# Performance work log

Measured on AMD Instinct MI355X. Metric: run time of the kernel, lower is better.

Reference implementation:

```python
import jax, jax.numpy as jnp
import numpy as np

N, E, DIN, DOUT = 50000, 800000, 256, 64
LN_EPS = 1e-5


def setup_inputs() -> dict:
    key = jax.random.key(0)
    k1, k2, k3 = jax.random.split(key, 3)
    xs = jax.random.normal(k1, (N, DIN), dtype=jnp.float32)
    edge_index = jax.random.randint(k2, (2, E), 0, N, dtype=jnp.int64)
    # GCNConv linear weight (glorot-ish) and bias
    W = jax.random.normal(k3, (DOUT, DIN), dtype=jnp.float32) * (1.0 / np.sqrt(DIN))
    b = jnp.zeros((DOUT,), dtype=jnp.float32)
    # LayerNorm affine params
    gamma = jnp.ones((DOUT,), dtype=jnp.float32)
    beta = jnp.zeros((DOUT,), dtype=jnp.float32)
    return {"xs": xs, "edge_index": edge_index, "W": W, "b": b, "gamma": gamma, "beta": beta}


def reference(xs, edge_index, W, b, gamma, beta):
    n = xs.shape[0]
    # 1) linear transform first (PyG GCNConv order): [N, DOUT]
    h = xs @ W.T
    # 2) add self loops
    loop = jnp.arange(n, dtype=edge_index.dtype)
    src = jnp.concatenate([edge_index[0], loop])
    dst = jnp.concatenate([edge_index[1], loop])
    # 3) symmetric normalization: deg over destinations (incl. self loops)
    deg = jax.ops.segment_sum(jnp.ones_like(dst, dtype=h.dtype), dst, num_segments=n)
    dinv = jnp.where(deg > 0, jax.lax.rsqrt(deg), 0.0)
    norm = dinv[src] * dinv[dst]  # [E+N]
    # 4) gather -> weight -> scatter-add
    msg = h[src] * norm[:, None]  # [E+N, DOUT]
    out = jax.ops.segment_sum(msg, dst, num_segments=n) + b
    # 5) LayerNorm over feature dim
    mu = jnp.mean(out, axis=-1, keepdims=True)
    var = jnp.mean(jnp.square(out - mu), axis=-1, keepdims=True)
    return (out - mu) * jax.lax.rsqrt(var + LN_EPS) * gamma + beta
```

## Files before the change

kernel.cpp:

```cpp
#include <hip/hip_runtime.h>

#define N_NODES 50000
#define N_EDGES 800000
#define DIN 256
#define DOUT 64
#define LN_EPS 1e-5f
#define NB 782
#define BCAP 2048
#define EPB 2048

typedef __attribute__((ext_vector_type(8))) short bfrag8;
typedef __attribute__((ext_vector_type(4))) float f32x4;

__device__ inline unsigned short f2bf(float f) {
    unsigned u = __builtin_bit_cast(unsigned, f);
    u += 0x7fffu + ((u >> 16) & 1u);
    return (unsigned short)(u >> 16);
}
__device__ inline float bf2f(unsigned short b) {
    unsigned u = ((unsigned)b) << 16;
    return __builtin_bit_cast(float, u);
}

__global__ void zero_gcur_kernel(int* __restrict__ gcur) {
    int i = blockIdx.x * 256 + threadIdx.x;
    if (i < NB) gcur[i] = 0;
}

__global__ __launch_bounds__(512) void partition_kernel(
    const int* __restrict__ ei, int* __restrict__ gcur, unsigned* __restrict__ bdata) {
    __shared__ int hist[NB];
    __shared__ int hbase[NB];
    const int tid = threadIdx.x;
    for (int c = tid; c < NB; c += 512) hist[c] = 0;
    __syncthreads();
    const int chunk = blockIdx.x * EPB;
    unsigned u[4];
    int bk[4];
    int rk[4];
    #pragma unroll
    for (int i = 0; i < 4; ++i) {
        int e = chunk + i * 512 + tid;
        if (e < N_EDGES) {
            int s = ei[e];
            int d = ei[N_EDGES + e];
            u[i] = (unsigned)s | ((unsigned)(d & 63) << 17);
            bk[i] = d >> 6;
            rk[i] = atomicAdd(&hist[bk[i]], 1);
        } else { bk[i] = -1; u[i] = 0; rk[i] = 0; }
    }
    __syncthreads();
    for (int c = tid; c < NB; c += 512) {
        int n = hist[c];
        hbase[c] = n ? atomicAdd(&gcur[c], n) : 0;
    }
    __syncthreads();
    #pragma unroll
    for (int i = 0; i < 4; ++i) {
        if (bk[i] >= 0) {
            int off = hbase[bk[i]] + rk[i];
            if (off < BCAP) bdata[(size_t)bk[i] * BCAP + off] = u[i];
        }
    }
}

__global__ __launch_bounds__(512) void sort_dinv_kernel(
    unsigned* __restrict__ bdata, const int* __restrict__ gcur,
    float* __restrict__ dinv, int* __restrict__ nstart, int* __restrict__ nend) {
    __shared__ unsigned buf[BCAP];
    __shared__ int hist[64];
    __shared__ int pre[64];
    const int tid = threadIdx.x, b = blockIdx.x;
    if (tid < 64) hist[tid] = 0;
    __syncthreads();
    int cntb = gcur[b];
    if (cntb > BCAP) cntb = BCAP;
    unsigned* bd = bdata + (size_t)b * BCAP;
    unsigned v[4];
    int rk[4];
    #pragma unroll
    for (int j = 0; j < 4; ++j) {
        int i = tid + j * 512;
        if (i < cntb) {
            v[j] = bd[i];
            rk[j] = atomicAdd(&hist[v[j] >> 17], 1);
        } else { v[j] = 0; rk[j] = -1; }
    }
    __syncthreads();
    if (tid < 64) {
        int n = hist[tid], s = n;
        #pragma unroll
        for (int d = 1; d < 64; d <<= 1) {
            int t = __shfl_up(s, d, 64);
            if (tid >= d) s += t;
        }
        pre[tid] = s - n;
        int node = b * 64 + tid;
        if (node < N_NODES) {
            dinv[node] = rsqrtf((float)(n + 1));
            nstart[node] = b * BCAP + (s - n);
            nend[node]   = b * BCAP + s;
        }
    }
    __syncthreads();
    #pragma unroll
    for (int j = 0; j < 4; ++j) {
        if (rk[j] >= 0)
            buf[pre[v[j] >> 17] + rk[j]] = v[j] & 0x1FFFF;
    }
    __syncthreads();
    #pragma unroll
    for (int j = 0; j < 4; ++j) {
        int i = tid + j * 512;
        if (i < cntb) bd[i] = buf[i];
    }
}

__global__ __launch_bounds__(512) void gemm_kernel(const float* __restrict__ xs,
                                                   const float* __restrict__ W,
                                                   const float* __restrict__ dinv,
                                                   unsigned short* __restrict__ hs) {
    __shared__ bfrag8 wg[64 * 32];
    const int tid = threadIdx.x;
    #pragma unroll
    for (int i = 0; i < 4; ++i) {
        int gi = tid + i * 512;
        int d = gi >> 5, g = gi & 31;
        const float* src = W + d * 256 + g * 8;
        f32x4 f0 = *(const f32x4*)src;
        f32x4 f1 = *(const f32x4*)(src + 4);
        union { unsigned short us[8]; bfrag8 v; } p;
        p.us[0] = f2bf(f0.x); p.us[1] = f2bf(f0.y);
        p.us[2] = f2bf(f0.z); p.us[3] = f2bf(f0.w);
        p.us[4] = f2bf(f1.x); p.us[5] = f2bf(f1.y);
        p.us[6] = f2bf(f1.z); p.us[7] = f2bf(f1.w);
        wg[d * 32 + (g ^ (d & 7))] = p.v;
    }
    __syncthreads();

    const int lane = tid & 63, wv = tid >> 6;
    const int n0 = (blockIdx.x * 8 + wv) * 16;
    int arow = n0 + (lane & 15);
    if (arow >= N_NODES) arow = N_NODES - 1;
    const float* xrow = xs + (size_t)arow * DIN + (lane >> 4) * 8;

    f32x4 acc[4] = {{0.f, 0.f, 0.f, 0.f}, {0.f, 0.f, 0.f, 0.f},
                    {0.f, 0.f, 0.f, 0.f}, {0.f, 0.f, 0.f, 0.f}};
    const int swz = lane & 7;
    #pragma unroll
    for (int s = 0; s < 8; ++s) {
        f32x4 xa = *(const f32x4*)(xrow + s * 32);
        f32x4 xb = *(const f32x4*)(xrow + s * 32 + 4);
        union { unsigned short us[8]; bfrag8 v; } a;
        a.us[0] = f2bf(xa.x); a.us[1] = f2bf(xa.y);
        a.us[2] = f2bf(xa.z); a.us[3] = f2bf(xa.w);
        a.us[4] = f2bf(xb.x); a.us[5] = f2bf(xb.y);
        a.us[6] = f2bf(xb.z); a.us[7] = f2bf(xb.w);
        int g = s * 4 + (lane >> 4);
        #pragma unroll
        for (int t = 0; t < 4; ++t) {
            bfrag8 b = wg[(t * 16 + (lane & 15)) * 32 + (g ^ swz)];
            acc[t] = __builtin_amdgcn_mfma_f32_16x16x32_bf16(a.v, b, acc[t], 0, 0, 0);
        }
    }
    #pragma unroll
    for (int t = 0; t < 4; ++t) {
        #pragma unroll
        for (int r = 0; r < 4; ++r) {
            int row = n0 + (lane >> 4) * 4 + r;
            if (row < N_NODES) {
                float dr = dinv[row];
                hs[(size_t)row * DOUT + t * 16 + (lane & 15)] = f2bf(acc[t][r] * dr);
            }
        }
    }
}

__global__ __launch_bounds__(256) void csr_agg_ln_kernel(
    const unsigned* __restrict__ csr, const int* __restrict__ nstart,
    const int* __restrict__ nend, const unsigned short* __restrict__ hs,
    const float* __restrict__ dinv, const float* __restrict__ bias,
    const float* __restrict__ gamma, const float* __restrict__ beta,
    float* __restrict__ out) {
    const int tid = threadIdx.x, lane = tid & 63, wv = tid >> 6;
    const int q = lane >> 4;
    const int fl = lane & 15;
    const int node = (blockIdx.x * 4 + wv) * 4 + q;
    if (node >= N_NODES) return;
    const int c0 = nstart[node];
    const int deg = nend[node] - c0;
    const int cmax = deg > 0 ? deg - 1 : 0;

    uint2 sv = *(const uint2*)(hs + (size_t)node * DOUT + fl * 4);
    float a0 = bf2f((unsigned short)(sv.x & 0xFFFFu));
    float a1 = bf2f((unsigned short)(sv.x >> 16));
    float a2 = bf2f((unsigned short)(sv.y & 0xFFFFu));
    float a3 = bf2f((unsigned short)(sv.y >> 16));

    int maxd = deg;
    maxd = max(maxd, __shfl_xor(maxd, 16, 64));
    maxd = max(maxd, __shfl_xor(maxd, 32, 64));

    for (int j = 0; j < maxd; j += 8) {
        unsigned uu[8];
        #pragma unroll
        for (int k = 0; k < 8; ++k) {
            int jc = j + k; jc = jc < cmax ? jc : cmax;
            uu[k] = csr[c0 + jc];
        }
        uint2 hv[8];
        #pragma unroll
        for (int k = 0; k < 8; ++k) {
            unsigned src = uu[k];
            if (src > (unsigned)(N_NODES - 1)) src = N_NODES - 1;
            hv[k] = *(const uint2*)(hs + (size_t)src * DOUT + fl * 4);
        }
        #pragma unroll
        for (int k = 0; k < 8; ++k) {
            bool valid = (j + k) < deg;
            unsigned x = valid ? hv[k].x : 0u;
            unsigned y = valid ? hv[k].y : 0u;
            a0 += bf2f((unsigned short)(x & 0xFFFFu));
            a1 += bf2f((unsigned short)(x >> 16));
            a2 += bf2f((unsigned short)(y & 0xFFFFu));
            a3 += bf2f((unsigned short)(y >> 16));
        }
    }
    float di = dinv[node];
    float4 b4  = ((const float4*)bias)[fl];
    float4 g4  = ((const float4*)gamma)[fl];
    float4 be4 = ((const float4*)beta)[fl];
    a0 = a0 * di + b4.x;
    a1 = a1 * di + b4.y;
    a2 = a2 * di + b4.z;
    a3 = a3 * di + b4.w;
    float sum = (a0 + a1) + (a2 + a3);
    #pragma unroll
    for (int d = 1; d < 16; d <<= 1) sum += __shfl_xor(sum, d, 64);
    float mu = sum * (1.0f / 64.0f);
    float d0 = a0 - mu, d1 = a1 - mu, d2 = a2 - mu, d3 = a3 - mu;
    float vs = (d0 * d0 + d1 * d1) + (d2 * d2 + d3 * d3);
    #pragma unroll
    for (int d = 1; d < 16; d <<= 1) vs += __shfl_xor(vs, d, 64);
    float var = vs * (1.0f / 64.0f);
    float rinv = rsqrtf(var + LN_EPS);
    float4 ov;
    ov.x = d0 * rinv * g4.x + be4.x;
    ov.y = d1 * rinv * g4.y + be4.y;
    ov.z = d2 * rinv * g4.z + be4.z;
    ov.w = d3 * rinv * g4.w + be4.w;
    *(float4*)(out + (size_t)node * DOUT + fl * 4) = ov;
}

extern "C" void kernel_launch(void* const* d_in, const int* in_sizes, int n_in,
                              void* d_out, int out_size, void* d_ws, size_t ws_size,
                              hipStream_t stream) {
    const float* xs    = (const float*)d_in[0];
    const int*   ei    = (const int*)d_in[1];
    const float* W     = (const float*)d_in[2];
    const float* bias  = (const float*)d_in[3];
    const float* gamma = (const float*)d_in[4];
    const float* beta  = (const float*)d_in[5];
    float* out = (float*)d_out;

    char* base = (char*)d_ws;
    auto align_up = [](size_t x) { return (x + 255) & ~(size_t)255; };
    size_t o = 0;
    int* gcur   = (int*)(base + o);      o = align_up(o + (size_t)NB * 4);
    float* dinv = (float*)(base + o);    o = align_up(o + (size_t)N_NODES * 4);
    unsigned* bdata = (unsigned*)(base + o);
    o = align_up(o + (size_t)NB * BCAP * 4);
    unsigned short* hs = (unsigned short*)(base + o);
    o = align_up(o + (size_t)N_NODES * DOUT * 2);
    int* nstart = (int*)(base + o);      o = align_up(o + (size_t)N_NODES * 4);
    int* nend   = (int*)(base + o);      o = align_up(o + (size_t)N_NODES * 4);
    (void)ws_size; (void)in_sizes; (void)n_in; (void)out_size;

    zero_gcur_kernel<<<(NB + 255) / 256, 256, 0, stream>>>(gcur);
    partition_kernel<<<(N_EDGES + EPB - 1) / EPB, 512, 0, stream>>>(ei, gcur, bdata);
    sort_dinv_kernel<<<NB, 512, 0, stream>>>(bdata, gcur, dinv, nstart, nend);
    gemm_kernel<<<(N_NODES + 127) / 128, 512, 0, stream>>>(xs, W, dinv, hs);
    csr_agg_ln_kernel<<<(N_NODES + 15) / 16, 256, 0, stream>>>(
        bdata, nstart, nend, hs, dinv, bias, gamma, beta, out);
}
```

Baseline: 61.23 us.

## Fuse all five stages into one cooperative persistent kernel with grid syncs

Replaces the five separate launches (zero, partition, sort/dinv, GEMM, CSR aggregate+LayerNorm) with a single cooperative kernel of 391 blocks that separates the stages with grid.sync(). Each block now sorts two buckets and the aggregation stage becomes a grid-stride loop over node groups. This is meant to remove the per-launch overhead and the gaps between kernels. In exchange it adds four grid-wide barriers, limits the aggregation to 391 blocks and caps occupancy through launch bounds and cooperative residency.

```diff
diff --git a/kernel.cpp b/kernel.cpp
--- a/kernel.cpp
+++ b/kernel.cpp
@@ -1,4 +1,7 @@
 #include <hip/hip_runtime.h>
+#include <hip/hip_cooperative_groups.h>
+
+namespace cg = cooperative_groups;
 
 #define N_NODES 50000
 #define N_EDGES 800000
@@ -7,6 +10,7 @@
 #define LN_EPS 1e-5f
 #define NB 782
 #define BCAP 2048
+#define GRID 391
 #define EPB 2048
 
 typedef __attribute__((ext_vector_type(8))) short bfrag8;
@@ -22,234 +26,235 @@
     return __builtin_bit_cast(float, u);
 }
 
-__global__ void zero_gcur_kernel(int* __restrict__ gcur) {
-    int i = blockIdx.x * 256 + threadIdx.x;
-    if (i < NB) gcur[i] = 0;
-}
-
-__global__ __launch_bounds__(512) void partition_kernel(
-    const int* __restrict__ ei, int* __restrict__ gcur, unsigned* __restrict__ bdata) {
-    __shared__ int hist[NB];
-    __shared__ int hbase[NB];
+__global__ __launch_bounds__(512, 4) void fused_kernel(
+    const float* __restrict__ xs, const int* __restrict__ ei,
+    const float* __restrict__ W, const float* __restrict__ bias,
+    const float* __restrict__ gamma, const float* __restrict__ beta,
+    int* __restrict__ gcur, float* __restrict__ dinv,
+    unsigned* __restrict__ bdata, unsigned short* __restrict__ hs,
+    int* __restrict__ nstart, int* __restrict__ nend, float* __restrict__ out) {
+    cg::grid_group grid = cg::this_grid();
+    __shared__ __align__(16) char smraw[32768];
     const int tid = threadIdx.x;
-    for (int c = tid; c < NB; c += 512) hist[c] = 0;
-    __syncthreads();
-    const int chunk = blockIdx.x * EPB;
-    unsigned u[4];
-    int bk[4];
-    int rk[4];
-    #pragma unroll
-    for (int i = 0; i < 4; ++i) {
-        int e = chunk + i * 512 + tid;
-        if (e < N_EDGES) {
-            int s = ei[e];
-            int d = ei[N_EDGES + e];
-            u[i] = (unsigned)s | ((unsigned)(d & 63) << 17);
-            bk[i] = d >> 6;
-            rk[i] = atomicAdd(&hist[bk[i]], 1);
-        } else { bk[i] = -1; u[i] = 0; rk[i] = 0; }
-    }
-    __syncthreads();
-    for (int c = tid; c < NB; c += 512) {
-        int n = hist[c];
-        hbase[c] = n ? atomicAdd(&gcur[c], n) : 0;
-    }
-    __syncthreads();
-    #pragma unroll
-    for (int i = 0; i < 4; ++i) {
-        if (bk[i] >= 0) {
-            int off = hbase[bk[i]] + rk[i];
-            if (off < BCAP) bdata[(size_t)bk[i] * BCAP + off] = u[i];
-        }
-    }
-}
-
-__global__ __launch_bounds__(512) void sort_dinv_kernel(
-    unsigned* __restrict__ bdata, const int* __restrict__ gcur,
-    float* __restrict__ dinv, int* __restrict__ nstart, int* __restrict__ nend) {
-    __shared__ unsigned buf[BCAP];
-    __shared__ int hist[64];
-    __shared__ int pre[64];
-    const int tid = threadIdx.x, b = blockIdx.x;
-    if (tid < 64) hist[tid] = 0;
-    __syncthreads();
-    int cntb = gcur[b];
-    if (cntb > BCAP) cntb = BCAP;
-    unsigned* bd = bdata + (size_t)b * BCAP;
-    unsigned v[4];
-    int rk[4];
-    #pragma unroll
-    for (int j = 0; j < 4; ++j) {
-        int i = tid + j * 512;
-        if (i < cntb) {
-            v[j] = bd[i];
-            rk[j] = atomicAdd(&hist[v[j] >> 17], 1);
-        } else { v[j] = 0; rk[j] = -1; }
-    }
-    __syncthreads();
-    if (tid < 64) {
-        int n = hist[tid], s = n;
-        #pragma unroll
-        for (int d = 1; d < 64; d <<= 1) {
-            int t = __shfl_up(s, d, 64);
-            if (tid >= d) s += t;
-        }
-        pre[tid] = s - n;
-        int node = b * 64 + tid;
-        if (node < N_NODES) {
-            dinv[node] = rsqrtf((float)(n + 1));
-            nstart[node] = b * BCAP + (s - n);
-            nend[node]   = b * BCAP + s;
-        }
-    }
-    __syncthreads();
-    #pragma unroll
-    for (int j = 0; j < 4; ++j) {
-        if (rk[j] >= 0)
-            buf[pre[v[j] >> 17] + rk[j]] = v[j] & 0x1FFFF;
-    }
-    __syncthreads();
-    #pragma unroll
-    for (int j = 0; j < 4; ++j) {
-        int i = tid + j * 512;
-        if (i < cntb) bd[i] = buf[i];
-    }
-}
-
-__global__ __launch_bounds__(512) void gemm_kernel(const float* __restrict__ xs,
-                                                   const float* __restrict__ W,
-                                                   const float* __restrict__ dinv,
-                                                   unsigned short* __restrict__ hs) {
-    __shared__ bfrag8 wg[64 * 32];
-    const int tid = threadIdx.x;
-    #pragma unroll
-    for (int i = 0; i < 4; ++i) {
-        int gi = tid + i * 512;
-        int d = gi >> 5, g = gi & 31;
-        const float* src = W + d * 256 + g * 8;
-        f32x4 f0 = *(const f32x4*)src;
-        f32x4 f1 = *(const f32x4*)(src + 4);
-        union { unsigned short us[8]; bfrag8 v; } p;
-        p.us[0] = f2bf(f0.x); p.us[1] = f2bf(f0.y);
-        p.us[2] = f2bf(f0.z); p.us[3] = f2bf(f0.w);
-        p.us[4] = f2bf(f1.x); p.us[5] = f2bf(f1.y);
-        p.us[6] = f2bf(f1.z); p.us[7] = f2bf(f1.w);
-        wg[d * 32 + (g ^ (d & 7))] = p.v;
-    }
-    __syncthreads();
-
-    const int lane = tid & 63, wv = tid >> 6;
-    const int n0 = (blockIdx.x * 8 + wv) * 16;
-    int arow = n0 + (lane & 15);
-    if (arow >= N_NODES) arow = N_NODES - 1;
-    const float* xrow = xs + (size_t)arow * DIN + (lane >> 4) * 8;
-
-    f32x4 acc[4] = {{0.f, 0.f, 0.f, 0.f}, {0.f, 0.f, 0.f, 0.f},
-                    {0.f, 0.f, 0.f, 0.f}, {0.f, 0.f, 0.f, 0.f}};
-    const int swz = lane & 7;
-    #pragma unroll
-    for (int s = 0; s < 8; ++s) {
-        f32x4 xa = *(const f32x4*)(xrow + s * 32);
-        f32x4 xb = *(const f32x4*)(xrow + s * 32 + 4);
-        union { unsigned short us[8]; bfrag8 v; } a;
-        a.us[0] = f2bf(xa.x); a.us[1] = f2bf(xa.y);
-        a.us[2] = f2bf(xa.z); a.us[3] = f2bf(xa.w);
-        a.us[4] = f2bf(xb.x); a.us[5] = f2bf(xb.y);
-        a.us[6] = f2bf(xb.z); a.us[7] = f2bf(xb.w);
-        int g = s * 4 + (lane >> 4);
+
+    {
+        int i = blockIdx.x * 512 + tid;
+        if (i < NB) gcur[i] = 0;
+    }
+    grid.sync();
+
+    {
+        int* hist  = (int*)smraw;
+        int* hbase = hist + NB;
+        for (int c = tid; c < NB; c += 512) hist[c] = 0;
+        __syncthreads();
+        const int chunk = blockIdx.x * EPB;
+        unsigned u[4]; int bk[4]; int rk[4];
+        #pragma unroll
+        for (int i = 0; i < 4; ++i) {
+            int e = chunk + i * 512 + tid;
+            if (e < N_EDGES) {
+                int s = ei[e];
+                int d = ei[N_EDGES + e];
+                u[i] = (unsigned)s | ((unsigned)(d & 63) << 17);
+                bk[i] = d >> 6;
+                rk[i] = atomicAdd(&hist[bk[i]], 1);
+            } else { bk[i] = -1; u[i] = 0; rk[i] = 0; }
+        }
+        __syncthreads();
+        for (int c = tid; c < NB; c += 512) {
+            int n = hist[c];
+            hbase[c] = n ? atomicAdd(&gcur[c], n) : 0;
+        }
+        __syncthreads();
+        #pragma unroll
+        for (int i = 0; i < 4; ++i) {
+            if (bk[i] >= 0) {
+                int off = hbase[bk[i]] + rk[i];
+                if (off < BCAP) bdata[(size_t)bk[i] * BCAP + off] = u[i];
+            }
+        }
+    }
+    grid.sync();
+
+    {
+        unsigned* buf = (unsigned*)smraw;
+        int* hist = (int*)(smraw + BCAP * 4);
+        int* pre  = hist + 64;
+        #pragma unroll
+        for (int t2 = 0; t2 < 2; ++t2) {
+            int b = blockIdx.x * 2 + t2;
+            if (tid < 64) hist[tid] = 0;
+            __syncthreads();
+            int cntb = gcur[b];
+            if (cntb > BCAP) cntb = BCAP;
+            unsigned* bd = bdata + (size_t)b * BCAP;
+            unsigned v[4]; int rk[4];
+            #pragma unroll
+            for (int j = 0; j < 4; ++j) {
+                int i = tid + j * 512;
+                if (i < cntb) {
+                    v[j] = bd[i];
+                    rk[j] = atomicAdd(&hist[v[j] >> 17], 1);
+                } else { v[j] = 0; rk[j] = -1; }
+            }
+            __syncthreads();
+            if (tid < 64) {
+                int n = hist[tid], s = n;
+                #pragma unroll
+                for (int d = 1; d < 64; d <<= 1) {
+                    int t = __shfl_up(s, d, 64);
+                    if (tid >= d) s += t;
+                }
+                pre[tid] = s - n;
+                int node = b * 64 + tid;
+                if (node < N_NODES) {
+                    dinv[node] = rsqrtf((float)(n + 1));
+                    nstart[node] = b * BCAP + (s - n);
+                    nend[node]   = b * BCAP + s;
+                }
+            }
+            __syncthreads();
+            #pragma unroll
+            for (int j = 0; j < 4; ++j) {
+                if (rk[j] >= 0)
+                    buf[pre[v[j] >> 17] + rk[j]] = v[j] & 0x1FFFF;
+            }
+            __syncthreads();
+            #pragma unroll
+            for (int j = 0; j < 4; ++j) {
+                int i = tid + j * 512;
+                if (i < cntb) bd[i] = buf[i];
+            }
+            __syncthreads();
+        }
+    }
+    grid.sync();
+
+    {
+        bfrag8* wg = (bfrag8*)smraw;
+        #pragma unroll
+        for (int i = 0; i < 4; ++i) {
+            int gi = tid + i * 512;
+            int d = gi >> 5, g = gi & 31;
+            const float* src = W + d * 256 + g * 8;
+            f32x4 f0 = *(const f32x4*)src;
+            f32x4 f1 = *(const f32x4*)(src + 4);
+            union { unsigned short us[8]; bfrag8 v; } p;
+            p.us[0] = f2bf(f0.x); p.us[1] = f2bf(f0.y);
+            p.us[2] = f2bf(f0.z); p.us[3] = f2bf(f0.w);
+            p.us[4] = f2bf(f1.x); p.us[5] = f2bf(f1.y);
+            p.us[6] = f2bf(f1.z); p.us[7] = f2bf(f1.w);
+            wg[d * 32 + (g ^ (d & 7))] = p.v;
+        }
+        __syncthreads();
+        const int lane = tid & 63, wv = tid >> 6;
+        const int n0 = (blockIdx.x * 8 + wv) * 16;
+        int arow = n0 + (lane & 15);
+        if (arow >= N_NODES) arow = N_NODES - 1;
+        const float* xrow = xs + (size_t)arow * DIN + (lane >> 4) * 8;
+        f32x4 acc[4] = {{0.f, 0.f, 0.f, 0.f}, {0.f, 0.f, 0.f, 0.f},
+                        {0.f, 0.f, 0.f, 0.f}, {0.f, 0.f, 0.f, 0.f}};
+        const int swz = lane & 7;
+        #pragma unroll
+        for (int s = 0; s < 8; ++s) {
+            f32x4 xa = *(const f32x4*)(xrow + s * 32);
+            f32x4 xb = *(const f32x4*)(xrow + s * 32 + 4);
+            union { unsigned short us[8]; bfrag8 v; } a;
+            a.us[0] = f2bf(xa.x); a.us[1] = f2bf(xa.y);
+            a.us[2] = f2bf(xa.z); a.us[3] = f2bf(xa.w);
+            a.us[4] = f2bf(xb.x); a.us[5] = f2bf(xb.y);
+            a.us[6] = f2bf(xb.z); a.us[7] = f2bf(xb.w);
+            int g = s * 4 + (lane >> 4);
+            #pragma unroll
+            for (int t = 0; t < 4; ++t) {
+                bfrag8 b = wg[(t * 16 + (lane & 15)) * 32 + (g ^ swz)];
+                acc[t] = __builtin_amdgcn_mfma_f32_16x16x32_bf16(a.v, b, acc[t], 0, 0, 0);
+            }
+        }
         #pragma unroll
         for (int t = 0; t < 4; ++t) {
-            bfrag8 b = wg[(t * 16 + (lane & 15)) * 32 + (g ^ swz)];
-            acc[t] = __builtin_amdgcn_mfma_f32_16x16x32_bf16(a.v, b, acc[t], 0, 0, 0);
-        }
-    }
-    #pragma unroll
-    for (int t = 0; t < 4; ++t) {
-        #pragma unroll
-        for (int r = 0; r < 4; ++r) {
-            int row = n0 + (lane >> 4) * 4 + r;
-            if (row < N_NODES) {
-                float dr = dinv[row];
-                hs[(size_t)row * DOUT + t * 16 + (lane & 15)] = f2bf(acc[t][r] * dr);
-            }
-        }
-    }
-}
-
-__global__ __launch_bounds__(256) void csr_agg_ln_kernel(
-    const unsigned* __restrict__ csr, const int* __restrict__ nstart,
-    const int* __restrict__ nend, const unsigned short* __restrict__ hs,
-    const float* __restrict__ dinv, const float* __restrict__ bias,
-    const float* __restrict__ gamma, const float* __restrict__ beta,
-    float* __restrict__ out) {
-    const int tid = threadIdx.x, lane = tid & 63, wv = tid >> 6;
-    const int q = lane >> 4;
-    const int fl = lane & 15;
-    const int node = (blockIdx.x * 4 + wv) * 4 + q;
-    if (node >= N_NODES) return;
-    const int c0 = nstart[node];
-    const int deg = nend[node] - c0;
-    const int cmax = deg > 0 ? deg - 1 : 0;
-
-    uint2 sv = *(const uint2*)(hs + (size_t)node * DOUT + fl * 4);
-    float a0 = bf2f((unsigned short)(sv.x & 0xFFFFu));
-    float a1 = bf2f((unsigned short)(sv.x >> 16));
-    float a2 = bf2f((unsigned short)(sv.y & 0xFFFFu));
-    float a3 = bf2f((unsigned short)(sv.y >> 16));
-
-    int maxd = deg;
-    maxd = max(maxd, __shfl_xor(maxd, 16, 64));
-    maxd = max(maxd, __shfl_xor(maxd, 32, 64));
-
-    for (int j = 0; j < maxd; j += 8) {
-        unsigned uu[8];
-        #pragma unroll
-        for (int k = 0; k < 8; ++k) {
-            int jc = j + k; jc = jc < cmax ? jc : cmax;
-            uu[k] = csr[c0 + jc];
-        }
-        uint2 hv[8];
-        #pragma unroll
-        for (int k = 0; k < 8; ++k) {
-            unsigned src = uu[k];
-            if (src > (unsigned)(N_NODES - 1)) src = N_NODES - 1;
-            hv[k] = *(const uint2*)(hs + (size_t)src * DOUT + fl * 4);
-        }
-        #pragma unroll
-        for (int k = 0; k < 8; ++k) {
-            bool valid = (j + k) < deg;
-            unsigned x = valid ? hv[k].x : 0u;
-            unsigned y = valid ? hv[k].y : 0u;
-            a0 += bf2f((unsigned short)(x & 0xFFFFu));
-            a1 += bf2f((unsigned short)(x >> 16));
-            a2 += bf2f((unsigned short)(y & 0xFFFFu));
-            a3 += bf2f((unsigned short)(y >> 16));
-        }
-    }
-    float di = dinv[node];
-    float4 b4  = ((const float4*)bias)[fl];
-    float4 g4  = ((const float4*)gamma)[fl];
-    float4 be4 = ((const float4*)beta)[fl];
-    a0 = a0 * di + b4.x;
-    a1 = a1 * di + b4.y;
-    a2 = a2 * di + b4.z;
-    a3 = a3 * di + b4.w;
-    float sum = (a0 + a1) + (a2 + a3);
-    #pragma unroll
-    for (int d = 1; d < 16; d <<= 1) sum += __shfl_xor(sum, d, 64);
-    float mu = sum * (1.0f / 64.0f);
-    float d0 = a0 - mu, d1 = a1 - mu, d2 = a2 - mu, d3 = a3 - mu;
-    float vs = (d0 * d0 + d1 * d1) + (d2 * d2 + d3 * d3);
-    #pragma unroll
-    for (int d = 1; d < 16; d <<= 1) vs += __shfl_xor(vs, d, 64);
-    float var = vs * (1.0f / 64.0f);
-    float rinv = rsqrtf(var + LN_EPS);
-    float4 ov;
-    ov.x = d0 * rinv * g4.x + be4.x;
-    ov.y = d1 * rinv * g4.y + be4.y;
-    ov.z = d2 * rinv * g4.z + be4.z;
-    ov.w = d3 * rinv * g4.w + be4.w;
-    *(float4*)(out + (size_t)node * DOUT + fl * 4) = ov;
+            #pragma unroll
+            for (int r = 0; r < 4; ++r) {
+                int row = n0 + (lane >> 4) * 4 + r;
+                if (row < N_NODES) {
+                    float dr = dinv[row];
+                    hs[(size_t)row * DOUT + t * 16 + (lane & 15)] = f2bf(acc[t][r] * dr);
+                }
+            }
+        }
+    }
+    grid.sync();
+
+    {
+        const int lane = tid & 63, wv = tid >> 6;
+        const int q = lane >> 4;
+        const int fl = lane & 15;
+        const int gw = blockIdx.x * 8 + wv;
+        for (int t = gw; t < 12500; t += GRID * 8) {
+            const int node = t * 4 + q;
+            const int c0 = nstart[node];
+            const int deg = nend[node] - c0;
+            const int cmax = deg > 0 ? deg - 1 : 0;
+            uint2 sv = *(const uint2*)(hs + (size_t)node * DOUT + fl * 4);
+            float a0 = bf2f((unsigned short)(sv.x & 0xFFFFu));
+            float a1 = bf2f((unsigned short)(sv.x >> 16));
+            float a2 = bf2f((unsigned short)(sv.y & 0xFFFFu));
+            float a3 = bf2f((unsigned short)(sv.y >> 16));
+            int maxd = deg;
+            maxd = max(maxd, __shfl_xor(maxd, 16, 64));
+            maxd = max(maxd, __shfl_xor(maxd, 32, 64));
+            for (int j = 0; j < maxd; j += 8) {
+                unsigned uu[8];
+                #pragma unroll
+                for (int k = 0; k < 8; ++k) {
+                    int jc = j + k; jc = jc < cmax ? jc : cmax;
+                    uu[k] = bdata[c0 + jc];
+                }
+                uint2 hv[8];
+                #pragma unroll
+                for (int k = 0; k < 8; ++k) {
+                    unsigned src = uu[k];
+                    if (src > (unsigned)(N_NODES - 1)) src = N_NODES - 1;
+                    hv[k] = *(const uint2*)(hs + (size_t)src * DOUT + fl * 4);
+                }
+                #pragma unroll
+                for (int k = 0; k < 8; ++k) {
+                    bool valid = (j + k) < deg;
+                    unsigned x = valid ? hv[k].x : 0u;
+                    unsigned y = valid ? hv[k].y : 0u;
+                    a0 += bf2f((unsigned short)(x & 0xFFFFu));
+                    a1 += bf2f((unsigned short)(x >> 16));
+                    a2 += bf2f((unsigned short)(y & 0xFFFFu));
+                    a3 += bf2f((unsigned short)(y >> 16));
+                }
+            }
+            float di = dinv[node];
+            float4 b4  = ((const float4*)bias)[fl];
+            float4 g4  = ((const float4*)gamma)[fl];
+            float4 be4 = ((const float4*)beta)[fl];
+            a0 = a0 * di + b4.x;
+            a1 = a1 * di + b4.y;
+            a2 = a2 * di + b4.z;
+            a3 = a3 * di + b4.w;
+            float sum = (a0 + a1) + (a2 + a3);
+            #pragma unroll
+            for (int d = 1; d < 16; d <<= 1) sum += __shfl_xor(sum, d, 64);
+            float mu = sum * (1.0f / 64.0f);
+            float d0 = a0 - mu, d1 = a1 - mu, d2 = a2 - mu, d3 = a3 - mu;
+            float vs = (d0 * d0 + d1 * d1) + (d2 * d2 + d3 * d3);
+            #pragma unroll
+            for (int d = 1; d < 16; d <<= 1) vs += __shfl_xor(vs, d, 64);
+            float var = vs * (1.0f / 64.0f);
+            float rinv = rsqrtf(var + LN_EPS);
+            float4 ov;
+            ov.x = d0 * rinv * g4.x + be4.x;
+            ov.y = d1 * rinv * g4.y + be4.y;
+            ov.z = d2 * rinv * g4.z + be4.z;
+            ov.w = d3 * rinv * g4.w + be4.w;
+            *(float4*)(out + (size_t)node * DOUT + fl * 4) = ov;
+        }
+    }
 }
 
 extern "C" void kernel_launch(void* const* d_in, const int* in_sizes, int n_in,
@@ -276,10 +281,10 @@
     int* nend   = (int*)(base + o);      o = align_up(o + (size_t)N_NODES * 4);
     (void)ws_size; (void)in_sizes; (void)n_in; (void)out_size;
 
-    zero_gcur_kernel<<<(NB + 255) / 256, 256, 0, stream>>>(gcur);
-    partition_kernel<<<(N_EDGES + EPB - 1) / EPB, 512, 0, stream>>>(ei, gcur, bdata);
-    sort_dinv_kernel<<<NB, 512, 0, stream>>>(bdata, gcur, dinv, nstart, nend);
-    gemm_kernel<<<(N_NODES + 127) / 128, 512, 0, stream>>>(xs, W, dinv, hs);
-    csr_agg_ln_kernel<<<(N_NODES + 15) / 16, 256, 0, stream>>>(
-        bdata, nstart, nend, hs, dinv, bias, gamma, beta, out);
-}
+    void* args[] = {(void*)&xs, (void*)&ei, (void*)&W, (void*)&bias,
+                    (void*)&gamma, (void*)&beta, (void*)&gcur, (void*)&dinv,
+                    (void*)&bdata, (void*)&hs, (void*)&nstart, (void*)&nend,
+                    (void*)&out};
+    hipLaunchCooperativeKernel((const void*)fused_kernel, dim3(GRID), dim3(512),
+                               args, 0, stream);
+}
```

New measurement: 244.4 us. 299% more time.

## Fuse edge partitioning and GEMM into one launch, apply source dinv in aggregation

Applied to the files above, without the earlier changes.

The edge partition and the dense GEMM now run as two halves of one grid, so the GEMM no longer waits on the degree computation. Because dinv is not known yet when the GEMM runs, the GEMM stores an unscaled h. The aggregation kernel instead loads dinv[src] for every gathered edge and scales the self term by dinv[node]. This removes one launch and lets the two memory-bound phases overlap, at the cost of an extra 4-byte gather per edge in the aggregation.

```diff
diff --git a/kernel.cpp b/kernel.cpp
--- a/kernel.cpp
+++ b/kernel.cpp
@@ -7,6 +7,7 @@
 #define LN_EPS 1e-5f
 #define NB 782
 #define BCAP 2048
+#define PBLK 391
 #define EPB 2048
 
 typedef __attribute__((ext_vector_type(8))) short bfrag8;
@@ -27,39 +28,93 @@
     if (i < NB) gcur[i] = 0;
 }
 
-__global__ __launch_bounds__(512) void partition_kernel(
-    const int* __restrict__ ei, int* __restrict__ gcur, unsigned* __restrict__ bdata) {
-    __shared__ int hist[NB];
-    __shared__ int hbase[NB];
+__global__ __launch_bounds__(512) void part_gemm_kernel(
+    const int* __restrict__ ei, int* __restrict__ gcur, unsigned* __restrict__ bdata,
+    const float* __restrict__ xs, const float* __restrict__ W,
+    unsigned short* __restrict__ h) {
+    __shared__ __align__(16) char smraw[32768];
     const int tid = threadIdx.x;
-    for (int c = tid; c < NB; c += 512) hist[c] = 0;
-    __syncthreads();
-    const int chunk = blockIdx.x * EPB;
-    unsigned u[4];
-    int bk[4];
-    int rk[4];
-    #pragma unroll
-    for (int i = 0; i < 4; ++i) {
-        int e = chunk + i * 512 + tid;
-        if (e < N_EDGES) {
-            int s = ei[e];
-            int d = ei[N_EDGES + e];
-            u[i] = (unsigned)s | ((unsigned)(d & 63) << 17);
-            bk[i] = d >> 6;
-            rk[i] = atomicAdd(&hist[bk[i]], 1);
-        } else { bk[i] = -1; u[i] = 0; rk[i] = 0; }
-    }
-    __syncthreads();
-    for (int c = tid; c < NB; c += 512) {
-        int n = hist[c];
-        hbase[c] = n ? atomicAdd(&gcur[c], n) : 0;
-    }
-    __syncthreads();
-    #pragma unroll
-    for (int i = 0; i < 4; ++i) {
-        if (bk[i] >= 0) {
-            int off = hbase[bk[i]] + rk[i];
-            if (off < BCAP) bdata[(size_t)bk[i] * BCAP + off] = u[i];
+    if (blockIdx.x < PBLK) {
+        int* hist  = (int*)smraw;
+        int* hbase = hist + NB;
+        for (int c = tid; c < NB; c += 512) hist[c] = 0;
+        __syncthreads();
+        const int chunk = blockIdx.x * EPB;
+        unsigned u[4]; int bk[4]; int rk[4];
+        #pragma unroll
+        for (int i = 0; i < 4; ++i) {
+            int e = chunk + i * 512 + tid;
+            if (e < N_EDGES) {
+                int s = ei[e];
+                int d = ei[N_EDGES + e];
+                u[i] = (unsigned)s | ((unsigned)(d & 63) << 17);
+                bk[i] = d >> 6;
+                rk[i] = atomicAdd(&hist[bk[i]], 1);
+            } else { bk[i] = -1; u[i] = 0; rk[i] = 0; }
+        }
+        __syncthreads();
+        for (int c = tid; c < NB; c += 512) {
+            int n = hist[c];
+            hbase[c] = n ? atomicAdd(&gcur[c], n) : 0;
+        }
+        __syncthreads();
+        #pragma unroll
+        for (int i = 0; i < 4; ++i) {
+            if (bk[i] >= 0) {
+                int off = hbase[bk[i]] + rk[i];
+                if (off < BCAP) bdata[(size_t)bk[i] * BCAP + off] = u[i];
+            }
+        }
+    } else {
+        bfrag8* wg = (bfrag8*)smraw;
+        #pragma unroll
+        for (int i = 0; i < 4; ++i) {
+            int gi = tid + i * 512;
+            int d = gi >> 5, g = gi & 31;
+            const float* src = W + d * 256 + g * 8;
+            f32x4 f0 = *(const f32x4*)src;
+            f32x4 f1 = *(const f32x4*)(src + 4);
+            union { unsigned short us[8]; bfrag8 v; } p;
+            p.us[0] = f2bf(f0.x); p.us[1] = f2bf(f0.y);
+            p.us[2] = f2bf(f0.z); p.us[3] = f2bf(f0.w);
+            p.us[4] = f2bf(f1.x); p.us[5] = f2bf(f1.y);
+            p.us[6] = f2bf(f1.z); p.us[7] = f2bf(f1.w);
+            wg[d * 32 + (g ^ (d & 7))] = p.v;
+        }
+        __syncthreads();
+        const int lane = tid & 63, wv = tid >> 6;
+        const int bid = blockIdx.x - PBLK;
+        const int n0 = (bid * 8 + wv) * 16;
+        int arow = n0 + (lane & 15);
+        if (arow >= N_NODES) arow = N_NODES - 1;
+        const float* xrow = xs + (size_t)arow * DIN + (lane >> 4) * 8;
+        f32x4 acc[4] = {{0.f, 0.f, 0.f, 0.f}, {0.f, 0.f, 0.f, 0.f},
+                        {0.f, 0.f, 0.f, 0.f}, {0.f, 0.f, 0.f, 0.f}};
+        const int swz = lane & 7;
+        #pragma unroll
+        for (int s = 0; s < 8; ++s) {
+            f32x4 xa = *(const f32x4*)(xrow + s * 32);
+            f32x4 xb = *(const f32x4*)(xrow + s * 32 + 4);
+            union { unsigned short us[8]; bfrag8 v; } a;
+            a.us[0] = f2bf(xa.x); a.us[1] = f2bf(xa.y);
+            a.us[2] = f2bf(xa.z); a.us[3] = f2bf(xa.w);
+            a.us[4] = f2bf(xb.x); a.us[5] = f2bf(xb.y);
+            a.us[6] = f2bf(xb.z); a.us[7] = f2bf(xb.w);
+            int g = s * 4 + (lane >> 4);
+            #pragma unroll
+            for (int t = 0; t < 4; ++t) {
+                bfrag8 b = wg[(t * 16 + (lane & 15)) * 32 + (g ^ swz)];
+                acc[t] = __builtin_amdgcn_mfma_f32_16x16x32_bf16(a.v, b, acc[t], 0, 0, 0);
+            }
+        }
+        #pragma unroll
+        for (int t = 0; t < 4; ++t) {
+            #pragma unroll
+            for (int r = 0; r < 4; ++r) {
+                int row = n0 + (lane >> 4) * 4 + r;
+                if (row < N_NODES)
+                    h[(size_t)row * DOUT + t * 16 + (lane & 15)] = f2bf(acc[t][r]);
+            }
         }
     }
 }
@@ -116,69 +171,9 @@
     }
 }
 
-__global__ __launch_bounds__(512) void gemm_kernel(const float* __restrict__ xs,
-                                                   const float* __restrict__ W,
-                                                   const float* __restrict__ dinv,
-                                                   unsigned short* __restrict__ hs) {
-    __shared__ bfrag8 wg[64 * 32];
-    const int tid = threadIdx.x;
-    #pragma unroll
-    for (int i = 0; i < 4; ++i) {
-        int gi = tid + i * 512;
-        int d = gi >> 5, g = gi & 31;
-        const float* src = W + d * 256 + g * 8;
-        f32x4 f0 = *(const f32x4*)src;
-        f32x4 f1 = *(const f32x4*)(src + 4);
-        union { unsigned short us[8]; bfrag8 v; } p;
-        p.us[0] = f2bf(f0.x); p.us[1] = f2bf(f0.y);
-        p.us[2] = f2bf(f0.z); p.us[3] = f2bf(f0.w);
-        p.us[4] = f2bf(f1.x); p.us[5] = f2bf(f1.y);
-        p.us[6] = f2bf(f1.z); p.us[7] = f2bf(f1.w);
-        wg[d * 32 + (g ^ (d & 7))] = p.v;
-    }
-    __syncthreads();
-
-    const int lane = tid & 63, wv = tid >> 6;
-    const int n0 = (blockIdx.x * 8 + wv) * 16;
-    int arow = n0 + (lane & 15);
-    if (arow >= N_NODES) arow = N_NODES - 1;
-    const float* xrow = xs + (size_t)arow * DIN + (lane >> 4) * 8;
-
-    f32x4 acc[4] = {{0.f, 0.f, 0.f, 0.f}, {0.f, 0.f, 0.f, 0.f},
-                    {0.f, 0.f, 0.f, 0.f}, {0.f, 0.f, 0.f, 0.f}};
-    const int swz = lane & 7;
-    #pragma unroll
-    for (int s = 0; s < 8; ++s) {
-        f32x4 xa = *(const f32x4*)(xrow + s * 32);
-        f32x4 xb = *(const f32x4*)(xrow + s * 32 + 4);
-        union { unsigned short us[8]; bfrag8 v; } a;
-        a.us[0] = f2bf(xa.x); a.us[1] = f2bf(xa.y);
-        a.us[2] = f2bf(xa.z); a.us[3] = f2bf(xa.w);
-        a.us[4] = f2bf(xb.x); a.us[5] = f2bf(xb.y);
-        a.us[6] = f2bf(xb.z); a.us[7] = f2bf(xb.w);
-        int g = s * 4 + (lane >> 4);
-        #pragma unroll
-        for (int t = 0; t < 4; ++t) {
-            bfrag8 b = wg[(t * 16 + (lane & 15)) * 32 + (g ^ swz)];
-            acc[t] = __builtin_amdgcn_mfma_f32_16x16x32_bf16(a.v, b, acc[t], 0, 0, 0);
-        }
-    }
-    #pragma unroll
-    for (int t = 0; t < 4; ++t) {
-        #pragma unroll
-        for (int r = 0; r < 4; ++r) {
-            int row = n0 + (lane >> 4) * 4 + r;
-            if (row < N_NODES) {
-                float dr = dinv[row];
-                hs[(size_t)row * DOUT + t * 16 + (lane & 15)] = f2bf(acc[t][r] * dr);
-            }
-        }
-    }
-}
-
 __global__ __launch_bounds__(256) void csr_agg_ln_kernel(
     const unsigned* __restrict__ csr, const int* __restrict__ nstart,
-    const int* __restrict__ nend, const unsigned short* __restrict__ hs,
+    const int* __restrict__ nend, const unsigned short* __restrict__ h,
     const float* __restrict__ dinv, const float* __restrict__ bias,
     const float* __restrict__ gamma, const float* __restrict__ beta,
     float* __restrict__ out) {
@@ -190,12 +185,13 @@
     const int c0 = nstart[node];
     const int deg = nend[node] - c0;
     const int cmax = deg > 0 ? deg - 1 : 0;
-
-    uint2 sv = *(const uint2*)(hs + (size_t)node * DOUT + fl * 4);
-    float a0 = bf2f((unsigned short)(sv.x & 0xFFFFu));
-    float a1 = bf2f((unsigned short)(sv.x >> 16));
-    float a2 = bf2f((unsigned short)(sv.y & 0xFFFFu));
-    float a3 = bf2f((unsigned short)(sv.y >> 16));
+    const float di = dinv[node];
+
+    uint2 sv = *(const uint2*)(h + (size_t)node * DOUT + fl * 4);
+    float a0 = bf2f((unsigned short)(sv.x & 0xFFFFu)) * di;
+    float a1 = bf2f((unsigned short)(sv.x >> 16)) * di;
+    float a2 = bf2f((unsigned short)(sv.y & 0xFFFFu)) * di;
+    float a3 = bf2f((unsigned short)(sv.y >> 16)) * di;
 
     int maxd = deg;
     maxd = max(maxd, __shfl_xor(maxd, 16, 64));
@@ -209,24 +205,25 @@
             uu[k] = csr[c0 + jc];
         }
         uint2 hv[8];
+        float w[8];
         #pragma unroll
         for (int k = 0; k < 8; ++k) {
             unsigned src = uu[k];
             if (src > (unsigned)(N_NODES - 1)) src = N_NODES - 1;
-            hv[k] = *(const uint2*)(hs + (size_t)src * DOUT + fl * 4);
+            hv[k] = *(const uint2*)(h + (size_t)src * DOUT + fl * 4);
+            w[k] = dinv[src];
         }
         #pragma unroll
         for (int k = 0; k < 8; ++k) {
             bool valid = (j + k) < deg;
             unsigned x = valid ? hv[k].x : 0u;
             unsigned y = valid ? hv[k].y : 0u;
-            a0 += bf2f((unsigned short)(x & 0xFFFFu));
-            a1 += bf2f((unsigned short)(x >> 16));
-            a2 += bf2f((unsigned short)(y & 0xFFFFu));
-            a3 += bf2f((unsigned short)(y >> 16));
-        }
-    }
-    float di = dinv[node];
+            a0 = fmaf(bf2f((unsigned short)(x & 0xFFFFu)), w[k], a0);
+            a1 = fmaf(bf2f((unsigned short)(x >> 16)), w[k], a1);
+            a2 = fmaf(bf2f((unsigned short)(y & 0xFFFFu)), w[k], a2);
+            a3 = fmaf(bf2f((unsigned short)(y >> 16)), w[k], a3);
+        }
+    }
     float4 b4  = ((const float4*)bias)[fl];
     float4 g4  = ((const float4*)gamma)[fl];
     float4 be4 = ((const float4*)beta)[fl];
@@ -270,16 +267,15 @@
     float* dinv = (float*)(base + o);    o = align_up(o + (size_t)N_NODES * 4);
     unsigned* bdata = (unsigned*)(base + o);
     o = align_up(o + (size_t)NB * BCAP * 4);
-    unsigned short* hs = (unsigned short*)(base + o);
+    unsigned short* h = (unsigned short*)(base + o);
     o = align_up(o + (size_t)N_NODES * DOUT * 2);
     int* nstart = (int*)(base + o);      o = align_up(o + (size_t)N_NODES * 4);
     int* nend   = (int*)(base + o);      o = align_up(o + (size_t)N_NODES * 4);
     (void)ws_size; (void)in_sizes; (void)n_in; (void)out_size;
 
     zero_gcur_kernel<<<(NB + 255) / 256, 256, 0, stream>>>(gcur);
-    partition_kernel<<<(N_EDGES + EPB - 1) / EPB, 512, 0, stream>>>(ei, gcur, bdata);
+    part_gemm_kernel<<<2 * PBLK, 512, 0, stream>>>(ei, gcur, bdata, xs, W, h);
     sort_dinv_kernel<<<NB, 512, 0, stream>>>(bdata, gcur, dinv, nstart, nend);
-    gemm_kernel<<<(N_NODES + 127) / 128, 512, 0, stream>>>(xs, W, dinv, hs);
     csr_agg_ln_kernel<<<(N_NODES + 15) / 16, 256, 0, stream>>>(
-        bdata, nstart, nend, hs, dinv, bias, gamma, beta, out);
-}
+        bdata, nstart, nend, h, dinv, bias, gamma, beta, out);
+}
```

Result: no change. 61.21 us (-0.0%).
